# Kernel optimization log

Measured on AMD Instinct MI355X. Metric: run time of the kernel, lower is better.

## Reference

```python
import jax, jax.numpy as jnp
import numpy as np

NX = 4096
NY = 4096
DX = 0.01
DY = 0.01
DT = 0.001
CX = 1.0
CY = 1.0
CXW = DT / DX / 2.0 * CX  # 0.05, x-direction stencil coefficient
CYW = DT / DY / 2.0 * CY  # 0.05, y-direction stencil coefficient
DIAG = 1.0                # A[1,1]
NLEVEL = int(np.log2(min(NX, NY))) + 1  # 13


def _smooth(x):
    # 3x3 cross-correlation with kernel A, valid padding (stride 1, no pad).
    # A[0,1]=CYW, A[2,1]=-CYW, A[1,0]=CXW, A[1,1]=1, A[1,2]=-CXW.
    return (CYW * x[:-2, 1:-1] - CYW * x[2:, 1:-1]
            + CXW * x[1:-1, :-2] + x[1:-1, 1:-1] - CXW * x[1:-1, 2:])


def _bc(u):
    # Replicate edges (not corners: corners stay exactly 0, as in the torch code).
    H, W = u.shape
    p = jnp.zeros((H + 2, W + 2), u.dtype)
    p = p.at[1:-1, 1:-1].set(u)
    p = p.at[0, 1:-1].set(u[0])
    p = p.at[-1, 1:-1].set(u[-1])
    p = p.at[1:-1, 0].set(u[:, 0])
    p = p.at[1:-1, -1].set(u[:, -1])
    return p


def _restrict(x):
    # 2x2 average pooling, stride 2 (conv weight = 0.25 everywhere).
    return 0.25 * (x[0::2, 0::2] + x[1::2, 0::2] + x[0::2, 1::2] + x[1::2, 1::2])


def _prolong(x):
    # Nearest-neighbor upsample by 2.
    return jnp.repeat(jnp.repeat(x, 2, axis=0), 2, axis=1)


def setup_inputs() -> dict:
    key = jax.random.key(0)
    u = jax.random.normal(key, (1, 1, NY, NX), dtype=jnp.float32)
    return {"u": u, "t": 4}


def reference(u, t):
    v = u[0, 0]  # (NY, NX)
    for _ in range(t):  # t outer F-cycle iterations (b = 0 source term)
        r = _smooth(_bc(v))  # residual on finest grid, (NY, NX)
        r_s = [r]
        for _i in range(1, NLEVEL - 3):
            r = _restrict(r)
            r_s.append(r)  # coarsest stored level is 8x8
        e = jnp.zeros((1, 1), v.dtype)
        for j in reversed(range(1, NLEVEL - 3)):
            # coarse-grid correction; broadcast of (small e) + r_s[j] matches torch
            e = e - _smooth(jnp.pad(e, 1)) / DIAG + r_s[j] / DIAG
            e = _prolong(e)
        v = v - e
        v = v - _smooth(_bc(v)) / DIAG
    return v[None, None]
```

## Files before the change

kernel.cpp:

```cpp
#include <hip/hip_runtime.h>
#include <cstddef>


constexpr float CW = 0.05f;

__device__ __forceinline__ float up_val(float Pc, float Pu, float Pd, float Pl,
                                        float Pr, float rv) {
  float sm = CW * Pu - CW * Pd + CW * Pl + Pc - CW * Pr;
  return (Pc - sm) + rv;
}

__global__ __launch_bounds__(256) void k_sr_chain(
    const float* __restrict__ v, float* __restrict__ r1,
    float* __restrict__ r2, float* __restrict__ r3,
    float* __restrict__ r4, float* __restrict__ r5) {
  const int n = 4096, h = 2048;
  __shared__ float r1s[64][65];
  __shared__ float r2s[32][33];
  __shared__ float r3s[16][17];
  __shared__ float r4s[8][9];
  int tid = threadIdx.x;
  int bx = blockIdx.x, by = blockIdx.y;
  int ty0 = by * 64, tx0 = bx * 64;

#pragma unroll
  for (int k = 0; k < 4; ++k) {
    int u = tid + 256 * k;
    int uy = u >> 5, ux = u & 31;
    int bi = (ty0 >> 1) + uy;
    int bj = (tx0 >> 1) + ux;
    int c0 = 4 * bj;
    int cl = max(c0 - 1, 0), cr = min(c0 + 4, n - 1);
    float a[6][6];
#pragma unroll
    for (int rr = 0; rr < 6; ++rr) {
      int R = min(max(4 * bi - 1 + rr, 0), n - 1);
      const float* row = v + (size_t)R * n;
      float4 m = *reinterpret_cast<const float4*>(row + c0);
      a[rr][0] = row[cl];
      a[rr][1] = m.x; a[rr][2] = m.y; a[rr][3] = m.z; a[rr][4] = m.w;
      a[rr][5] = row[cr];
    }
#pragma unroll
    for (int oi = 0; oi < 2; ++oi) {
      float2 o;
#pragma unroll
      for (int oj = 0; oj < 2; ++oj) {
        float s[2][2];
#pragma unroll
        for (int p = 0; p < 2; ++p)
#pragma unroll
          for (int q = 0; q < 2; ++q) {
            int P = 2 * oi + p, Q = 2 * oj + q;
            s[p][q] = CW * a[P][Q + 1] - CW * a[P + 2][Q + 1]
                    + CW * a[P + 1][Q] + a[P + 1][Q + 1] - CW * a[P + 1][Q + 2];
          }
        float val = 0.25f * (((s[0][0] + s[1][0]) + s[0][1]) + s[1][1]);
        (oj ? o.y : o.x) = val;
        r1s[2 * uy + oi][2 * ux + oj] = val;
      }
      *reinterpret_cast<float2*>(r1 + (size_t)(2 * bi + oi) * h + 2 * bj) = o;
    }
  }
  __syncthreads();

#pragma unroll
  for (int k = 0; k < 4; ++k) {
    int idx = tid + 256 * k;
    int I = idx >> 5, J = idx & 31;
    float val = 0.25f * (((r1s[2 * I][2 * J] + r1s[2 * I + 1][2 * J])
                          + r1s[2 * I][2 * J + 1]) + r1s[2 * I + 1][2 * J + 1]);
    r2s[I][J] = val;
    r2[(size_t)(32 * by + I) * 1024 + 32 * bx + J] = val;
  }
  __syncthreads();

  {
    int I = tid >> 4, J = tid & 15;
    float val = 0.25f * (((r2s[2 * I][2 * J] + r2s[2 * I + 1][2 * J])
                          + r2s[2 * I][2 * J + 1]) + r2s[2 * I + 1][2 * J + 1]);
    r3s[I][J] = val;
    r3[(size_t)(16 * by + I) * 512 + 16 * bx + J] = val;
  }
  __syncthreads();

  if (tid < 64) {
    int I = tid >> 3, J = tid & 7;
    float val = 0.25f * (((r3s[2 * I][2 * J] + r3s[2 * I + 1][2 * J])
                          + r3s[2 * I][2 * J + 1]) + r3s[2 * I + 1][2 * J + 1]);
    r4s[I][J] = val;
    r4[(size_t)(8 * by + I) * 256 + 8 * bx + J] = val;
  }
  __syncthreads();

  if (tid < 16) {
    int I = tid >> 2, J = tid & 3;
    float val = 0.25f * (((r4s[2 * I][2 * J] + r4s[2 * I + 1][2 * J])
                          + r4s[2 * I][2 * J + 1]) + r4s[2 * I + 1][2 * J + 1]);
    r5[(size_t)(4 * by + I) * 128 + 4 * bx + J] = val;
  }
}

__global__ __launch_bounds__(1024, 1) void k_coarse_ext(
    const float* __restrict__ r5, const float* __restrict__ r4,
    float* __restrict__ E4) {
  __shared__ float r5s[128 * 128];
  __shared__ float r6s[64 * 64];
  __shared__ float r7s[32 * 32];
  __shared__ float r8s[16 * 16];
  __shared__ float r9s[8 * 8];
  __shared__ float E8s[16 * 16];
  __shared__ float E7s[32 * 32];
  __shared__ float E6s[64 * 64];
  __shared__ float e5r[10][128];
  int tid = threadIdx.x;
  int bid = blockIdx.x;

  auto up_lds = [&](const float* Ep, const float* rr, int i, int c, int nn) {
    int ss = nn >> 1;
    float Pc = Ep[(i >> 1) * ss + (c >> 1)];
    float Pu = (i > 0)      ? Ep[((i - 1) >> 1) * ss + (c >> 1)] : 0.0f;
    float Pd = (i < nn - 1) ? Ep[((i + 1) >> 1) * ss + (c >> 1)] : 0.0f;
    float Pl = (c > 0)      ? Ep[(i >> 1) * ss + ((c - 1) >> 1)] : 0.0f;
    float Pr = (c < nn - 1) ? Ep[(i >> 1) * ss + ((c + 1) >> 1)] : 0.0f;
    return up_val(Pc, Pu, Pd, Pl, Pr, rr[i * nn + c]);
  };

  for (int idx = tid; idx < 4096; idx += 1024)
    reinterpret_cast<float4*>(r5s)[idx] = reinterpret_cast<const float4*>(r5)[idx];
  __syncthreads();
  for (int idx = tid; idx < 64 * 64; idx += 1024) {
    int I = idx >> 6, J = idx & 63;
    float a = r5s[(2 * I) * 128 + 2 * J],     b = r5s[(2 * I + 1) * 128 + 2 * J];
    float c = r5s[(2 * I) * 128 + 2 * J + 1], d = r5s[(2 * I + 1) * 128 + 2 * J + 1];
    r6s[idx] = 0.25f * (((a + b) + c) + d);
  }
  __syncthreads();
  if (tid < 32 * 32) {
    int I = tid >> 5, J = tid & 31;
    float a = r6s[(2 * I) * 64 + 2 * J],     b = r6s[(2 * I + 1) * 64 + 2 * J];
    float c = r6s[(2 * I) * 64 + 2 * J + 1], d = r6s[(2 * I + 1) * 64 + 2 * J + 1];
    r7s[tid] = 0.25f * (((a + b) + c) + d);
  }
  __syncthreads();
  if (tid < 16 * 16) {
    int I = tid >> 4, J = tid & 15;
    float a = r7s[(2 * I) * 32 + 2 * J],     b = r7s[(2 * I + 1) * 32 + 2 * J];
    float c = r7s[(2 * I) * 32 + 2 * J + 1], d = r7s[(2 * I + 1) * 32 + 2 * J + 1];
    r8s[tid] = 0.25f * (((a + b) + c) + d);
  }
  __syncthreads();
  if (tid < 8 * 8) {
    int I = tid >> 3, J = tid & 7;
    float a = r8s[(2 * I) * 16 + 2 * J],     b = r8s[(2 * I + 1) * 16 + 2 * J];
    float c = r8s[(2 * I) * 16 + 2 * J + 1], d = r8s[(2 * I + 1) * 16 + 2 * J + 1];
    r9s[tid] = 0.25f * (((a + b) + c) + d);
  }
  __syncthreads();
  if (tid < 16 * 16)
    E8s[tid] = up_lds(r9s, r8s, tid >> 4, tid & 15, 16);
  __syncthreads();
  if (tid < 32 * 32)
    E7s[tid] = up_lds(E8s, r7s, tid >> 5, tid & 31, 32);
  __syncthreads();
  for (int idx = tid; idx < 64 * 64; idx += 1024)
    E6s[idx] = up_lds(E7s, r6s, idx >> 6, idx & 63, 64);
  __syncthreads();
  for (int idx = tid; idx < 10 * 128; idx += 1024) {
    int t = idx >> 7, c = idx & 127;
    int i = min(max(8 * bid - 1 + t, 0), 127);
    e5r[t][c] = up_lds(E6s, r5s, i, c, 128);
  }
  __syncthreads();
  for (int idx = tid; idx < 16 * 256; idx += 1024) {
    int gi = 16 * bid + (idx >> 8);
    int gc = idx & 255;
    float Pc = e5r[(gi >> 1) - 8 * bid + 1][gc >> 1];
    float Pu = (gi > 0)   ? e5r[((gi - 1) >> 1) - 8 * bid + 1][gc >> 1] : 0.0f;
    float Pd = (gi < 255) ? e5r[((gi + 1) >> 1) - 8 * bid + 1][gc >> 1] : 0.0f;
    float Pl = (gc > 0)   ? e5r[(gi >> 1) - 8 * bid + 1][(gc - 1) >> 1] : 0.0f;
    float Pr = (gc < 255) ? e5r[(gi >> 1) - 8 * bid + 1][(gc + 1) >> 1] : 0.0f;
    E4[(size_t)gi * 256 + gc] = up_val(Pc, Pu, Pd, Pl, Pr, r4[(size_t)gi * 256 + gc]);
  }
}

__global__ __launch_bounds__(256) void k_up_e3e2(
    const float* __restrict__ E4, const float* __restrict__ r3,
    const float* __restrict__ r2, float* __restrict__ E2) {
  __shared__ float e3s[34][35];
  int tid = threadIdx.x;
  int bx = blockIdx.x, by = blockIdx.y;
  int br0 = 32 * by - 1, bc0 = 32 * bx - 1;

  for (int idx = tid; idx < 34 * 34; idx += 256) {
    int er = idx / 34, ec = idx % 34;
    int gr = br0 + er, gc = bc0 + ec;
    float val = 0.0f;
    if (gr >= 0 && gr < 512 && gc >= 0 && gc < 512) {
      float Pc = E4[(size_t)(gr >> 1) * 256 + (gc >> 1)];
      float Pu = (gr > 0)   ? E4[(size_t)((gr - 1) >> 1) * 256 + (gc >> 1)] : 0.0f;
      float Pd = (gr < 511) ? E4[(size_t)((gr + 1) >> 1) * 256 + (gc >> 1)] : 0.0f;
      float Pl = (gc > 0)   ? E4[(size_t)(gr >> 1) * 256 + ((gc - 1) >> 1)] : 0.0f;
      float Pr = (gc < 511) ? E4[(size_t)(gr >> 1) * 256 + ((gc + 1) >> 1)] : 0.0f;
      val = up_val(Pc, Pu, Pd, Pl, Pr, r3[(size_t)gr * 512 + gc]);
    }
    e3s[er][ec] = val;
  }
  __syncthreads();

#pragma unroll
  for (int k = 0; k < 4; ++k) {
    int u = tid + 256 * k;
    int rr = u >> 4, f = u & 15;
    int gR = 64 * by + rr;
    int gC = 64 * bx + 4 * f;
    int rc = (gR >> 1) - br0;
    int ru = ((gR - 1) >> 1) - br0;
    int rd = ((gR + 1) >> 1) - br0;
    float4 rv = *reinterpret_cast<const float4*>(r2 + (size_t)gR * 1024 + gC);
    float4 o;
#pragma unroll
    for (int q = 0; q < 4; ++q) {
      int c = gC + q;
      int lc = (c >> 1) - bc0;
      float Pc = e3s[rc][lc];
      float Pu = (gR > 0)    ? e3s[ru][lc] : 0.0f;
      float Pd = (gR < 1023) ? e3s[rd][lc] : 0.0f;
      float Pl = (c > 0)     ? e3s[rc][((c - 1) >> 1) - bc0] : 0.0f;
      float Pr = (c < 1023)  ? e3s[rc][((c + 1) >> 1) - bc0] : 0.0f;
      (&o.x)[q] = up_val(Pc, Pu, Pd, Pl, Pr, (&rv.x)[q]);
    }
    *reinterpret_cast<float4*>(E2 + (size_t)gR * 1024 + gC) = o;
  }
}

__global__ __launch_bounds__(256) void k_up(
    const float* __restrict__ Ep, const float* __restrict__ r,
    float* __restrict__ Eo, int n) {
  int s = n >> 1;
  int j = blockIdx.x * blockDim.x + threadIdx.x;
  int i = blockIdx.y * blockDim.y + threadIdx.y;
  if (i >= s || j >= (n >> 2)) return;
  const float* ec = Ep + (size_t)i * s + 2 * j;
  float epc0 = ec[0], epc1 = ec[1];
  float epl = (j > 0) ? ec[-1] : 0.0f;
  float epr = (2 * j + 2 < s) ? ec[2] : 0.0f;
  float epu0 = 0.0f, epu1 = 0.0f, epd0 = 0.0f, epd1 = 0.0f;
  if (i > 0)     { epu0 = ec[-s]; epu1 = ec[-s + 1]; }
  if (i < s - 1) { epd0 = ec[s];  epd1 = ec[s + 1]; }
  {
    float4 rv = *reinterpret_cast<const float4*>(r + (size_t)(2 * i) * n + 4 * j);
    float4 o;
    o.x = up_val(epc0, epu0, epc0, epl,  epc0, rv.x);
    o.y = up_val(epc0, epu0, epc0, epc0, epc1, rv.y);
    o.z = up_val(epc1, epu1, epc1, epc0, epc1, rv.z);
    o.w = up_val(epc1, epu1, epc1, epc1, epr,  rv.w);
    *reinterpret_cast<float4*>(Eo + (size_t)(2 * i) * n + 4 * j) = o;
  }
  {
    float4 rv = *reinterpret_cast<const float4*>(r + (size_t)(2 * i + 1) * n + 4 * j);
    float4 o;
    o.x = up_val(epc0, epc0, epd0, epl,  epc0, rv.x);
    o.y = up_val(epc0, epc0, epd0, epc0, epc1, rv.y);
    o.z = up_val(epc1, epc1, epd1, epc0, epc1, rv.z);
    o.w = up_val(epc1, epc1, epd1, epc1, epr,  rv.w);
    *reinterpret_cast<float4*>(Eo + (size_t)(2 * i + 1) * n + 4 * j) = o;
  }
}

__global__ __launch_bounds__(256) void k_final(
    const float* __restrict__ v, const float* __restrict__ E1,
    float* __restrict__ out) {
  const int n = 4096, h = 2048;
  int J = blockIdx.x * blockDim.x + threadIdx.x;
  int i = blockIdx.y * blockDim.y + threadIdx.y;
  int c0 = 4 * J;
  int cl = max(c0 - 1, 0), cr = min(c0 + 4, n - 1);
  int ecl = cl >> 1, ecr = cr >> 1;

  float e[3][4];
  int ers0 = max(2 * i - 1, 0) >> 1;
  int ers2 = min(2 * i + 2, n - 1) >> 1;
  const int ers[3] = {ers0, i, ers2};
#pragma unroll
  for (int t = 0; t < 3; ++t) {
    const float* erow = E1 + (size_t)ers[t] * h;
    e[t][0] = erow[ecl];
    e[t][1] = erow[2 * J];
    e[t][2] = erow[2 * J + 1];
    e[t][3] = erow[ecr];
  }

  float w[4][6];
  const int tmap[4] = {0, 1, 1, 2};
#pragma unroll
  for (int rr = 0; rr < 4; ++rr) {
    int R = min(max(2 * i - 1 + rr, 0), n - 1);
    int t = tmap[rr];
    const float* vrow = v + (size_t)R * n;
    float4 m = *reinterpret_cast<const float4*>(vrow + c0);
    w[rr][0] = vrow[cl] - e[t][0];
    w[rr][1] = m.x - e[t][1];
    w[rr][2] = m.y - e[t][1];
    w[rr][3] = m.z - e[t][2];
    w[rr][4] = m.w - e[t][2];
    w[rr][5] = vrow[cr] - e[t][3];
  }
#pragma unroll
  for (int a = 0; a < 2; ++a) {
    float4 o;
#pragma unroll
    for (int qq = 0; qq < 4; ++qq) {
      float ce = w[a + 1][qq + 1];
      float sm = CW * w[a][qq + 1] - CW * w[a + 2][qq + 1]
               + CW * w[a + 1][qq] + ce - CW * w[a + 1][qq + 2];
      (&o.x)[qq] = ce - sm;
    }
    *reinterpret_cast<float4*>(out + (size_t)(2 * i + a) * n + c0) = o;
  }
}

extern "C" void kernel_launch(void* const* d_in, const int* in_sizes, int n_in,
                              void* d_out, int out_size, void* d_ws, size_t ws_size,
                              hipStream_t stream) {
  (void)in_sizes; (void)n_in; (void)out_size;
  float* u = (float*)d_in[0];
  float* out = (float*)d_out;
  char* ws = (char*)d_ws;

  size_t off = 0;
  auto alloc = [&](size_t elems) {
    float* p = (float*)(ws + off);
    off += (elems * sizeof(float) + 255) & ~(size_t)255;
    return p;
  };
  float* r1 = alloc(2048 * 2048);
  float* r2 = alloc(1024 * 1024);
  float* r3 = alloc(512 * 512);
  float* r4 = alloc(256 * 256);
  float* r5 = alloc(128 * 128);
  float* E4 = alloc(256 * 256);
  float* E2 = alloc(1024 * 1024);
  float* E1 = alloc(2048 * 2048);
  size_t pool = off;
  const size_t VB = (size_t)4096 * 4096 * sizeof(float);
  bool big = ws_size >= pool + VB;
  float* vws = (float*)(ws + pool);

  dim3 b(64, 4);
  auto iterate = [&](const float* vin, float* vout) {
    k_sr_chain<<<dim3(32, 32), 256, 0, stream>>>(vin, r1, r2, r3, r4, r5);
    k_coarse_ext<<<16, 1024, 0, stream>>>(r5, r4, E4);
    k_up_e3e2<<<dim3(16, 16), 256, 0, stream>>>(E4, r3, r2, E2);
    k_up<<<dim3(8, 256), b, 0, stream>>>(E2, r1, E1, 2048);
    k_final<<<dim3(16, 512), b, 0, stream>>>(vin, E1, vout);
  };

  if (big) {
    iterate(u, vws);
    iterate(vws, out);
    iterate(out, vws);
    iterate(vws, out);
  } else {
    iterate(u, out);
    iterate(out, u);
    iterate(u, out);
    iterate(out, u);
    hipMemcpyAsync(out, u, VB, hipMemcpyDeviceToDevice, stream);
  }
}
```

Before: 380.4 us.

## Fuse coarse-grid correction into mid kernel and fold E1 prolongation into final

Merges the coarse-level solve, the E4/E3 prolongation and the E2 computation into one 256-block kernel that redundantly recomputes the coarse hierarchy per block. It also folds the E1 level into the final kernel by computing a tile of E1 in shared memory from E2 and r1. This removes two launches and the E4/E1 global round-trips, in particular the 16MB E1 write and read. In exchange each of the 256 blocks repeats the whole 128x128 coarse chain, where 16 blocks did before, and the final kernel gains a shared-memory staging step with a barrier.

```diff
diff --git a/kernel.cpp b/kernel.cpp
--- a/kernel.cpp
+++ b/kernel.cpp
@@ -101,9 +101,10 @@
   }
 }
 
-__global__ __launch_bounds__(1024, 1) void k_coarse_ext(
+__global__ __launch_bounds__(256, 1) void k_mid(
     const float* __restrict__ r5, const float* __restrict__ r4,
-    float* __restrict__ E4) {
+    const float* __restrict__ r3, const float* __restrict__ r2,
+    float* __restrict__ E2) {
   __shared__ float r5s[128 * 128];
   __shared__ float r6s[64 * 64];
   __shared__ float r7s[32 * 32];
@@ -113,8 +114,10 @@
   __shared__ float E7s[32 * 32];
   __shared__ float E6s[64 * 64];
   __shared__ float e5r[10][128];
+  __shared__ float e4s[18][20];
+  __shared__ float e3s[34][35];
   int tid = threadIdx.x;
-  int bid = blockIdx.x;
+  int bx = blockIdx.x, by = blockIdx.y;
 
   auto up_lds = [&](const float* Ep, const float* rr, int i, int c, int nn) {
     int ss = nn >> 1;
@@ -126,21 +129,21 @@
     return up_val(Pc, Pu, Pd, Pl, Pr, rr[i * nn + c]);
   };
 
-  for (int idx = tid; idx < 4096; idx += 1024)
+  for (int idx = tid; idx < 4096; idx += 256)
     reinterpret_cast<float4*>(r5s)[idx] = reinterpret_cast<const float4*>(r5)[idx];
   __syncthreads();
-  for (int idx = tid; idx < 64 * 64; idx += 1024) {
+  for (int idx = tid; idx < 64 * 64; idx += 256) {
     int I = idx >> 6, J = idx & 63;
     float a = r5s[(2 * I) * 128 + 2 * J],     b = r5s[(2 * I + 1) * 128 + 2 * J];
     float c = r5s[(2 * I) * 128 + 2 * J + 1], d = r5s[(2 * I + 1) * 128 + 2 * J + 1];
     r6s[idx] = 0.25f * (((a + b) + c) + d);
   }
   __syncthreads();
-  if (tid < 32 * 32) {
-    int I = tid >> 5, J = tid & 31;
+  for (int idx = tid; idx < 32 * 32; idx += 256) {
+    int I = idx >> 5, J = idx & 31;
     float a = r6s[(2 * I) * 64 + 2 * J],     b = r6s[(2 * I + 1) * 64 + 2 * J];
     float c = r6s[(2 * I) * 64 + 2 * J + 1], d = r6s[(2 * I + 1) * 64 + 2 * J + 1];
-    r7s[tid] = 0.25f * (((a + b) + c) + d);
+    r7s[idx] = 0.25f * (((a + b) + c) + d);
   }
   __syncthreads();
   if (tid < 16 * 16) {
@@ -163,51 +166,45 @@
   if (tid < 32 * 32)
     E7s[tid] = up_lds(E8s, r7s, tid >> 5, tid & 31, 32);
   __syncthreads();
-  for (int idx = tid; idx < 64 * 64; idx += 1024)
+  for (int idx = tid; idx < 64 * 64; idx += 256)
     E6s[idx] = up_lds(E7s, r6s, idx >> 6, idx & 63, 64);
   __syncthreads();
-  for (int idx = tid; idx < 10 * 128; idx += 1024) {
+  for (int idx = tid; idx < 10 * 128; idx += 256) {
     int t = idx >> 7, c = idx & 127;
-    int i = min(max(8 * bid - 1 + t, 0), 127);
+    int i = min(max(8 * by - 1 + t, 0), 127);
     e5r[t][c] = up_lds(E6s, r5s, i, c, 128);
   }
   __syncthreads();
-  for (int idx = tid; idx < 16 * 256; idx += 1024) {
-    int gi = 16 * bid + (idx >> 8);
-    int gc = idx & 255;
-    float Pc = e5r[(gi >> 1) - 8 * bid + 1][gc >> 1];
-    float Pu = (gi > 0)   ? e5r[((gi - 1) >> 1) - 8 * bid + 1][gc >> 1] : 0.0f;
-    float Pd = (gi < 255) ? e5r[((gi + 1) >> 1) - 8 * bid + 1][gc >> 1] : 0.0f;
-    float Pl = (gc > 0)   ? e5r[(gi >> 1) - 8 * bid + 1][(gc - 1) >> 1] : 0.0f;
-    float Pr = (gc < 255) ? e5r[(gi >> 1) - 8 * bid + 1][(gc + 1) >> 1] : 0.0f;
-    E4[(size_t)gi * 256 + gc] = up_val(Pc, Pu, Pd, Pl, Pr, r4[(size_t)gi * 256 + gc]);
-  }
-}
-
-__global__ __launch_bounds__(256) void k_up_e3e2(
-    const float* __restrict__ E4, const float* __restrict__ r3,
-    const float* __restrict__ r2, float* __restrict__ E2) {
-  __shared__ float e3s[34][35];
-  int tid = threadIdx.x;
-  int bx = blockIdx.x, by = blockIdx.y;
-  int br0 = 32 * by - 1, bc0 = 32 * bx - 1;
-
+  for (int idx = tid; idx < 18 * 18; idx += 256) {
+    int er = idx / 18, ec = idx % 18;
+    int ga = 16 * by - 1 + er, gb = 16 * bx - 1 + ec;
+    if (ga >= 0 && ga < 256 && gb >= 0 && gb < 256) {
+      float Pc = e5r[(ga >> 1) - (8 * by - 1)][gb >> 1];
+      float Pu = (ga > 0)   ? e5r[((ga - 1) >> 1) - (8 * by - 1)][gb >> 1] : 0.0f;
+      float Pd = (ga < 255) ? e5r[((ga + 1) >> 1) - (8 * by - 1)][gb >> 1] : 0.0f;
+      float Pl = (gb > 0)   ? e5r[(ga >> 1) - (8 * by - 1)][(gb - 1) >> 1] : 0.0f;
+      float Pr = (gb < 255) ? e5r[(ga >> 1) - (8 * by - 1)][(gb + 1) >> 1] : 0.0f;
+      e4s[er][ec] = up_val(Pc, Pu, Pd, Pl, Pr, r4[(size_t)ga * 256 + gb]);
+    }
+  }
+  __syncthreads();
   for (int idx = tid; idx < 34 * 34; idx += 256) {
     int er = idx / 34, ec = idx % 34;
-    int gr = br0 + er, gc = bc0 + ec;
+    int gr = 32 * by - 1 + er, gc = 32 * bx - 1 + ec;
     float val = 0.0f;
     if (gr >= 0 && gr < 512 && gc >= 0 && gc < 512) {
-      float Pc = E4[(size_t)(gr >> 1) * 256 + (gc >> 1)];
-      float Pu = (gr > 0)   ? E4[(size_t)((gr - 1) >> 1) * 256 + (gc >> 1)] : 0.0f;
-      float Pd = (gr < 511) ? E4[(size_t)((gr + 1) >> 1) * 256 + (gc >> 1)] : 0.0f;
-      float Pl = (gc > 0)   ? E4[(size_t)(gr >> 1) * 256 + ((gc - 1) >> 1)] : 0.0f;
-      float Pr = (gc < 511) ? E4[(size_t)(gr >> 1) * 256 + ((gc + 1) >> 1)] : 0.0f;
+      int e4r0 = 16 * by - 1, e4c0 = 16 * bx - 1;
+      float Pc = e4s[(gr >> 1) - e4r0][(gc >> 1) - e4c0];
+      float Pu = (gr > 0)   ? e4s[((gr - 1) >> 1) - e4r0][(gc >> 1) - e4c0] : 0.0f;
+      float Pd = (gr < 511) ? e4s[((gr + 1) >> 1) - e4r0][(gc >> 1) - e4c0] : 0.0f;
+      float Pl = (gc > 0)   ? e4s[(gr >> 1) - e4r0][((gc - 1) >> 1) - e4c0] : 0.0f;
+      float Pr = (gc < 511) ? e4s[(gr >> 1) - e4r0][((gc + 1) >> 1) - e4c0] : 0.0f;
       val = up_val(Pc, Pu, Pd, Pl, Pr, r3[(size_t)gr * 512 + gc]);
     }
     e3s[er][ec] = val;
   }
   __syncthreads();
-
+  int br0 = 32 * by - 1, bc0 = 32 * bx - 1;
 #pragma unroll
   for (int k = 0; k < 4; ++k) {
     int u = tid + 256 * k;
@@ -234,46 +231,32 @@
   }
 }
 
-__global__ __launch_bounds__(256) void k_up(
-    const float* __restrict__ Ep, const float* __restrict__ r,
-    float* __restrict__ Eo, int n) {
-  int s = n >> 1;
-  int j = blockIdx.x * blockDim.x + threadIdx.x;
-  int i = blockIdx.y * blockDim.y + threadIdx.y;
-  if (i >= s || j >= (n >> 2)) return;
-  const float* ec = Ep + (size_t)i * s + 2 * j;
-  float epc0 = ec[0], epc1 = ec[1];
-  float epl = (j > 0) ? ec[-1] : 0.0f;
-  float epr = (2 * j + 2 < s) ? ec[2] : 0.0f;
-  float epu0 = 0.0f, epu1 = 0.0f, epd0 = 0.0f, epd1 = 0.0f;
-  if (i > 0)     { epu0 = ec[-s]; epu1 = ec[-s + 1]; }
-  if (i < s - 1) { epd0 = ec[s];  epd1 = ec[s + 1]; }
-  {
-    float4 rv = *reinterpret_cast<const float4*>(r + (size_t)(2 * i) * n + 4 * j);
-    float4 o;
-    o.x = up_val(epc0, epu0, epc0, epl,  epc0, rv.x);
-    o.y = up_val(epc0, epu0, epc0, epc0, epc1, rv.y);
-    o.z = up_val(epc1, epu1, epc1, epc0, epc1, rv.z);
-    o.w = up_val(epc1, epu1, epc1, epc1, epr,  rv.w);
-    *reinterpret_cast<float4*>(Eo + (size_t)(2 * i) * n + 4 * j) = o;
-  }
-  {
-    float4 rv = *reinterpret_cast<const float4*>(r + (size_t)(2 * i + 1) * n + 4 * j);
-    float4 o;
-    o.x = up_val(epc0, epc0, epd0, epl,  epc0, rv.x);
-    o.y = up_val(epc0, epc0, epd0, epc0, epc1, rv.y);
-    o.z = up_val(epc1, epc1, epd1, epc0, epc1, rv.z);
-    o.w = up_val(epc1, epc1, epd1, epc1, epr,  rv.w);
-    *reinterpret_cast<float4*>(Eo + (size_t)(2 * i + 1) * n + 4 * j) = o;
-  }
-}
-
 __global__ __launch_bounds__(256) void k_final(
-    const float* __restrict__ v, const float* __restrict__ E1,
-    float* __restrict__ out) {
-  const int n = 4096, h = 2048;
-  int J = blockIdx.x * blockDim.x + threadIdx.x;
-  int i = blockIdx.y * blockDim.y + threadIdx.y;
+    const float* __restrict__ v, const float* __restrict__ E2,
+    const float* __restrict__ r1, float* __restrict__ out) {
+  const int n = 4096, h = 2048, s2 = 1024;
+  __shared__ float e1s[6][132];
+  int tx = threadIdx.x, ty = threadIdx.y;
+  int tid = ty * 64 + tx;
+  int bx = blockIdx.x, by = blockIdx.y;
+  int er0 = 4 * by - 1;
+  int ec0 = 128 * bx - 1;
+
+  for (int idx = tid; idx < 6 * 130; idx += 256) {
+    int lr = idx / 130, lc = idx % 130;
+    int a = min(max(er0 + lr, 0), h - 1);
+    int b = min(max(ec0 + lc, 0), h - 1);
+    float Pc = E2[(size_t)(a >> 1) * s2 + (b >> 1)];
+    float Pu = (a > 0)     ? E2[(size_t)((a - 1) >> 1) * s2 + (b >> 1)] : 0.0f;
+    float Pd = (a < h - 1) ? E2[(size_t)((a + 1) >> 1) * s2 + (b >> 1)] : 0.0f;
+    float Pl = (b > 0)     ? E2[(size_t)(a >> 1) * s2 + ((b - 1) >> 1)] : 0.0f;
+    float Pr = (b < h - 1) ? E2[(size_t)(a >> 1) * s2 + ((b + 1) >> 1)] : 0.0f;
+    e1s[lr][lc] = up_val(Pc, Pu, Pd, Pl, Pr, r1[(size_t)a * h + b]);
+  }
+  __syncthreads();
+
+  int J = bx * 64 + tx;
+  int i = by * 4 + ty;
   int c0 = 4 * J;
   int cl = max(c0 - 1, 0), cr = min(c0 + 4, n - 1);
   int ecl = cl >> 1, ecr = cr >> 1;
@@ -284,11 +267,11 @@
   const int ers[3] = {ers0, i, ers2};
 #pragma unroll
   for (int t = 0; t < 3; ++t) {
-    const float* erow = E1 + (size_t)ers[t] * h;
-    e[t][0] = erow[ecl];
-    e[t][1] = erow[2 * J];
-    e[t][2] = erow[2 * J + 1];
-    e[t][3] = erow[ecr];
+    const float* erow = e1s[ers[t] - er0];
+    e[t][0] = erow[ecl - ec0];
+    e[t][1] = erow[2 * J - ec0];
+    e[t][2] = erow[2 * J + 1 - ec0];
+    e[t][3] = erow[ecr - ec0];
   }
 
   float w[4][6];
@@ -339,21 +322,16 @@
   float* r3 = alloc(512 * 512);
   float* r4 = alloc(256 * 256);
   float* r5 = alloc(128 * 128);
-  float* E4 = alloc(256 * 256);
   float* E2 = alloc(1024 * 1024);
-  float* E1 = alloc(2048 * 2048);
   size_t pool = off;
   const size_t VB = (size_t)4096 * 4096 * sizeof(float);
   bool big = ws_size >= pool + VB;
   float* vws = (float*)(ws + pool);
 
-  dim3 b(64, 4);
   auto iterate = [&](const float* vin, float* vout) {
     k_sr_chain<<<dim3(32, 32), 256, 0, stream>>>(vin, r1, r2, r3, r4, r5);
-    k_coarse_ext<<<16, 1024, 0, stream>>>(r5, r4, E4);
-    k_up_e3e2<<<dim3(16, 16), 256, 0, stream>>>(E4, r3, r2, E2);
-    k_up<<<dim3(8, 256), b, 0, stream>>>(E2, r1, E1, 2048);
-    k_final<<<dim3(16, 512), b, 0, stream>>>(vin, E1, vout);
+    k_mid<<<dim3(16, 16), 256, 0, stream>>>(r5, r4, r3, r2, E2);
+    k_final<<<dim3(16, 512), dim3(64, 4), 0, stream>>>(vin, E2, r1, vout);
   };
 
   if (big) {
```

After: 419.4 us. 10.3% more time.
